# Kernel optimization log

Hardware: AMD Instinct MI355X
Metric: run time of the kernel (lower is better)

Reference implementation:

```python
import jax, jax.numpy as jnp
import numpy as np
from jax.scipy.stats import norm
from jax.scipy.special import ndtri

B, S, F = 512, 2048, 128

def setup_inputs() -> dict:
    key = jax.random.key(0)
    k1, k2, k3 = jax.random.split(key, 3)
    x = jax.random.normal(k1, (B, F), dtype=jnp.float32)
    cdf_data = jax.random.normal(k2, (S, F), dtype=jnp.float32)
    bw_param = jax.random.uniform(k3, (1, F), dtype=jnp.float32)
    return {"x": x, "cdf_data": cdf_data, "bw_param": bw_param}

def reference(x, cdf_data, bw_param):
    # trainable bandwidths: bw = sigmoid(raw param), shape [1, F]
    bw = jax.nn.sigmoid(bw_param)[0]  # [F]
    # Pairwise Gaussian-CDF KDE: for each (b, f), mean over stored samples s of
    # Phi((x[b,f] - cdf_data[s,f]) / bw[f]).  Intermediate z: [B, S, F].
    z = (x[:, None, :] - cdf_data[None, :, :]) / bw  # [B, S, F]
    u = jnp.mean(norm.cdf(z), axis=1)               # [B, F], uniform-ish in (0,1)
    # normal_backtransform=True: map uniform -> standard normal via inverse CDF
    return ndtri(u)
```

## Files before the change

kernel.cpp:

```cpp
#include <hip/hip_runtime.h>
#include <math.h>

#define FDIM  128
#define SDIM  2048
#define BDIM  512
#define GPTS  32
#define SP    32
#define PARTS 2
#define BLOCK1 (FDIM * PARTS)
#define XMIN  (-6.0)
#define XSPAN (12.0)
#define FG    2
#define BG    128
#define BLOCK2 256
#define PERF  (SP * GPTS)

__device__ __forceinline__ double ndtri_pair(double u, double cu) {
    double q = u - 0.5;
    if (fabs(q) <= 0.425) {
        double r = 0.180625 - q * q;
        double num = (((((((2.5090809287301226727e3  * r + 3.3430575583588128105e4) * r +
                            6.7265770927008700853e4) * r + 4.5921953931549871457e4) * r +
                            1.3731693765509461125e4) * r + 1.9715909503065514427e3) * r +
                            1.3314166789178437745e2) * r + 3.3871328727963666080e0);
        double den = (((((((5.2264952788528545610e3  * r + 2.8729085735721942674e4) * r +
                            3.9307895800092710610e4) * r + 2.1213794301586595867e4) * r +
                            5.3941960214247511077e3) * r + 6.8718700749205790830e2) * r +
                            4.2313330701600911252e1) * r + 1.0);
        return q * num / den;
    }
    double r = (q < 0.0) ? u : cu;
    r = fmax(r, 1e-300);
    r = sqrt(-log(r));
    double val;
    if (r <= 5.0) {
        r -= 1.6;
        double num = (((((((7.74545014278341407640e-4 * r + 2.27238449892691845833e-2) * r +
                            2.41780725177450611770e-1) * r + 1.27045825245236838258e0) * r +
                            3.64784832476320460504e0)  * r + 5.76949722146069140550e0) * r +
                            4.63033784615654529590e0)  * r + 1.42343711074968357734e0);
        double den = (((((((1.05075007164441684324e-9 * r + 5.47593808499534494600e-4) * r +
                            1.51986665636164571966e-2) * r + 1.48103976427480074590e-1) * r +
                            6.89767334985100004550e-1) * r + 1.67638483018380384940e0) * r +
                            2.05319162663775882187e0)  * r + 1.0);
        val = num / den;
    } else {
        r -= 5.0;
        double num = (((((((2.01033439929228813265e-7 * r + 2.71155556874348757815e-5) * r +
                            1.24266094738807843860e-3) * r + 2.65321895265761230930e-2) * r +
                            2.96560571828504891230e-1) * r + 1.78482653991729133580e0) * r +
                            5.46378491116411436990e0)  * r + 6.65790464350110377720e0);
        double den = (((((((2.04426310338993978564e-15 * r + 1.42151175831644588870e-7) * r +
                            1.84631831751005468180e-5)  * r + 7.86869131145613259100e-4) * r +
                            1.48753612908506148525e-2)  * r + 1.36929880922735805310e-1) * r +
                            5.99832206555887937690e-1)  * r + 1.0);
        val = num / den;
    }
    return (q < 0.0) ? -val : val;
}

__global__ __launch_bounds__(BLOCK1) void build_kernel(
    const float* __restrict__ cdf, const float* __restrict__ bwp,
    float2* __restrict__ part2)
{
    const int g    = blockIdx.x >> 5;
    const int sp   = blockIdx.x & (SP - 1);
    const int f    = threadIdx.x & (FDIM - 1);
    const int part = threadIdx.x >> 7;

    const float p = bwp[f];
    const float s = (1.0f + __expf(-p)) * 0.70710678118654752f;
    const float c1s    = 0.3275911f * s;
    const float negs2l = -(s * s) * 1.4426950408889634f;
    const float xg = (float)(XMIN + (double)g * (XSPAN / (GPTS - 1)));

    const int chunk = SDIM / SP / PARTS;
    const int base  = sp * (SDIM / SP) + part * chunk;
    const float* cp = cdf + base * FDIM + f;

    float acc0 = 0.f, acc1 = 0.f, acc2 = 0.f, acc3 = 0.f;
    float dac = 0.f;

    #pragma unroll 2
    for (int i = 0; i < chunk; i += 4) {
        float c0 = cp[0 * FDIM];
        float c1 = cp[1 * FDIM];
        float c2 = cp[2 * FDIM];
        float c3 = cp[3 * FDIM];
        cp += 4 * FDIM;

        float d0 = xg - c0, d1 = xg - c1, d2 = xg - c2, d3 = xg - c3;

        float t0 = __builtin_amdgcn_rcpf(fmaf(c1s, fabsf(d0), 1.0f));
        float t1 = __builtin_amdgcn_rcpf(fmaf(c1s, fabsf(d1), 1.0f));
        float t2 = __builtin_amdgcn_rcpf(fmaf(c1s, fabsf(d2), 1.0f));
        float t3 = __builtin_amdgcn_rcpf(fmaf(c1s, fabsf(d3), 1.0f));

        float x0 = exp2f(d0 * d0 * negs2l);
        float x1 = exp2f(d1 * d1 * negs2l);
        float x2 = exp2f(d2 * d2 * negs2l);
        float x3 = exp2f(d3 * d3 * negs2l);

        float q0 = fmaf(0.53070271450f, t0, -0.72657601350f);
        float q1 = fmaf(0.53070271450f, t1, -0.72657601350f);
        float q2 = fmaf(0.53070271450f, t2, -0.72657601350f);
        float q3 = fmaf(0.53070271450f, t3, -0.72657601350f);
        q0 = fmaf(q0, t0, 0.71070687050f);  q1 = fmaf(q1, t1, 0.71070687050f);
        q2 = fmaf(q2, t2, 0.71070687050f);  q3 = fmaf(q3, t3, 0.71070687050f);
        q0 = fmaf(q0, t0, -0.14224836800f); q1 = fmaf(q1, t1, -0.14224836800f);
        q2 = fmaf(q2, t2, -0.14224836800f); q3 = fmaf(q3, t3, -0.14224836800f);
        q0 = fmaf(q0, t0, 0.12741479600f);  q1 = fmaf(q1, t1, 0.12741479600f);
        q2 = fmaf(q2, t2, 0.12741479600f);  q3 = fmaf(q3, t3, 0.12741479600f);

        float e0 = q0 * t0 * x0;
        float e1 = q1 * t1 * x1;
        float e2 = q2 * t2 * x2;
        float e3 = q3 * t3 * x3;

        acc0 += (d0 >= 0.f) ? (1.0f - e0) : e0;
        acc1 += (d1 >= 0.f) ? (1.0f - e1) : e1;
        acc2 += (d2 >= 0.f) ? (1.0f - e2) : e2;
        acc3 += (d3 >= 0.f) ? (1.0f - e3) : e3;
        dac  += (x0 + x1) + (x2 + x3);
    }

    __shared__ float sacc[PARTS][FDIM];
    __shared__ float sdac[PARTS][FDIM];
    sacc[part][f] = (acc0 + acc1) + (acc2 + acc3);
    sdac[part][f] = dac;
    __syncthreads();

    if (part == 0) {
        float a  = sacc[0][f] + sacc[1][f];
        float da = sdac[0][f] + sdac[1][f];
        part2[f * PERF + sp * GPTS + g] = make_float2(a, da);
    }
}

__global__ __launch_bounds__(BLOCK2) void interp_kernel(
    const float* __restrict__ x, const float* __restrict__ bwp,
    const float2* __restrict__ part2, float* __restrict__ out)
{
    const int fg = blockIdx.x & 63;
    const int bg = blockIdx.x >> 6;
    const int F0 = fg * FG;
    const int B0 = bg * BG;
    const int tid = threadIdx.x;

    __shared__ float2 sp2[FG * PERF];
    __shared__ double tab[FG * GPTS][3];

    const float2* src = part2 + (size_t)F0 * PERF;
    #pragma unroll
    for (int k = tid; k < FG * PERF; k += BLOCK2) sp2[k] = src[k];
    __syncthreads();

    if (tid < FG * GPTS) {
        const int fi = tid >> 5;
        const int g  = tid & (GPTS - 1);
        double a = 0.0, da = 0.0;
        const int base = fi * PERF + g;
        #pragma unroll
        for (int sp = 0; sp < SP; ++sp) {
            float2 v = sp2[base + sp * GPTS];
            a  += (double)v.x;
            da += (double)v.y;
        }
        const double invS = 1.0 / (double)SDIM;
        const double invbw = 1.0 + exp(-(double)bwp[F0 + fi]);
        tab[tid][0] = a * invS;
        tab[tid][1] = ((double)SDIM - a) * invS;
        tab[tid][2] = da * invbw * (invS / 2.5066282746310002);
    }
    __syncthreads();

    const int bl = tid >> 1;
    const int fi = tid & 1;
    const int idx = (B0 + bl) * FDIM + F0 + fi;

    const double H = XSPAN / (GPTS - 1);
    double t = ((double)x[idx] - XMIN) * ((GPTS - 1) / XSPAN);
    t = fmin(fmax(t, 0.0), (double)(GPTS - 1));
    int i = (int)t;
    if (i > GPTS - 2) i = GPTS - 2;
    double w = t - (double)i;

    const int r0 = fi * GPTS + i;
    double u0 = tab[r0][0], u1 = tab[r0 + 1][0];
    double c0 = tab[r0][1], c1 = tab[r0 + 1][1];
    double m0 = tab[r0][2], m1 = tab[r0 + 1][2];

    double w2 = w * w, w3 = w2 * w;
    double h00 = 2.0 * w3 - 3.0 * w2 + 1.0;
    double h10 = w3 - 2.0 * w2 + w;
    double h01 = 3.0 * w2 - 2.0 * w3;
    double h11 = w3 - w2;
    double dterm = H * (h10 * m0 + h11 * m1);
    double u  = h00 * u0 + h01 * u1 + dterm;
    double cu = h00 * c0 + h01 * c1 - dterm;

    out[idx] = (float)ndtri_pair(u, cu);
}

extern "C" void kernel_launch(void* const* d_in, const int* in_sizes, int n_in,
                              void* d_out, int out_size, void* d_ws, size_t ws_size,
                              hipStream_t stream) {
    const float* x   = (const float*)d_in[0];
    const float* cdf = (const float*)d_in[1];
    const float* bwp = (const float*)d_in[2];
    float* out = (float*)d_out;

    float2* part2 = (float2*)d_ws;

    build_kernel<<<dim3(GPTS * SP), dim3(BLOCK1), 0, stream>>>(cdf, bwp, part2);
    interp_kernel<<<dim3((FDIM / FG) * (BDIM / BG)), dim3(BLOCK2), 0, stream>>>(
        x, bwp, part2, out);
}
```

Baseline: 67.11 us.

## Fuse build and interp kernels into one cooperative kernel with grid sync

```diff
diff --git a/kernel.cpp b/kernel.cpp
--- a/kernel.cpp
+++ b/kernel.cpp
@@ -1,19 +1,23 @@
 #include <hip/hip_runtime.h>
+#include <hip/hip_cooperative_groups.h>
 #include <math.h>
+
+namespace cg = cooperative_groups;
 
 #define FDIM  128
 #define SDIM  2048
 #define BDIM  512
 #define GPTS  32
-#define SP    32
+#define SPC   8
 #define PARTS 2
-#define BLOCK1 (FDIM * PARTS)
+#define CHUNK (SDIM / SPC / PARTS)
+#define NBLK  256
+#define NT    256
 #define XMIN  (-6.0)
 #define XSPAN (12.0)
 #define FG    2
 #define BG    128
-#define BLOCK2 256
-#define PERF  (SP * GPTS)
+#define PERF2 (SPC * GPTS)
 
 __device__ __forceinline__ double ndtri_pair(double u, double cu) {
     double q = u - 0.5;
@@ -59,110 +63,114 @@
     return (q < 0.0) ? -val : val;
 }
 
-__global__ __launch_bounds__(BLOCK1) void build_kernel(
-    const float* __restrict__ cdf, const float* __restrict__ bwp,
-    float2* __restrict__ part2)
+__global__ __launch_bounds__(NT) void fused_kernel(
+    const float* __restrict__ x, const float* __restrict__ cdf,
+    const float* __restrict__ bwp, float* out)
 {
-    const int g    = blockIdx.x >> 5;
-    const int sp   = blockIdx.x & (SP - 1);
-    const int f    = threadIdx.x & (FDIM - 1);
-    const int part = threadIdx.x >> 7;
-
-    const float p = bwp[f];
-    const float s = (1.0f + __expf(-p)) * 0.70710678118654752f;
-    const float c1s    = 0.3275911f * s;
-    const float negs2l = -(s * s) * 1.4426950408889634f;
-    const float xg = (float)(XMIN + (double)g * (XSPAN / (GPTS - 1)));
-
-    const int chunk = SDIM / SP / PARTS;
-    const int base  = sp * (SDIM / SP) + part * chunk;
-    const float* cp = cdf + base * FDIM + f;
-
-    float acc0 = 0.f, acc1 = 0.f, acc2 = 0.f, acc3 = 0.f;
-    float dac = 0.f;
-
-    #pragma unroll 2
-    for (int i = 0; i < chunk; i += 4) {
-        float c0 = cp[0 * FDIM];
-        float c1 = cp[1 * FDIM];
-        float c2 = cp[2 * FDIM];
-        float c3 = cp[3 * FDIM];
-        cp += 4 * FDIM;
-
-        float d0 = xg - c0, d1 = xg - c1, d2 = xg - c2, d3 = xg - c3;
-
-        float t0 = __builtin_amdgcn_rcpf(fmaf(c1s, fabsf(d0), 1.0f));
-        float t1 = __builtin_amdgcn_rcpf(fmaf(c1s, fabsf(d1), 1.0f));
-        float t2 = __builtin_amdgcn_rcpf(fmaf(c1s, fabsf(d2), 1.0f));
-        float t3 = __builtin_amdgcn_rcpf(fmaf(c1s, fabsf(d3), 1.0f));
-
-        float x0 = exp2f(d0 * d0 * negs2l);
-        float x1 = exp2f(d1 * d1 * negs2l);
-        float x2 = exp2f(d2 * d2 * negs2l);
-        float x3 = exp2f(d3 * d3 * negs2l);
-
-        float q0 = fmaf(0.53070271450f, t0, -0.72657601350f);
-        float q1 = fmaf(0.53070271450f, t1, -0.72657601350f);
-        float q2 = fmaf(0.53070271450f, t2, -0.72657601350f);
-        float q3 = fmaf(0.53070271450f, t3, -0.72657601350f);
-        q0 = fmaf(q0, t0, 0.71070687050f);  q1 = fmaf(q1, t1, 0.71070687050f);
-        q2 = fmaf(q2, t2, 0.71070687050f);  q3 = fmaf(q3, t3, 0.71070687050f);
-        q0 = fmaf(q0, t0, -0.14224836800f); q1 = fmaf(q1, t1, -0.14224836800f);
-        q2 = fmaf(q2, t2, -0.14224836800f); q3 = fmaf(q3, t3, -0.14224836800f);
-        q0 = fmaf(q0, t0, 0.12741479600f);  q1 = fmaf(q1, t1, 0.12741479600f);
-        q2 = fmaf(q2, t2, 0.12741479600f);  q3 = fmaf(q3, t3, 0.12741479600f);
-
-        float e0 = q0 * t0 * x0;
-        float e1 = q1 * t1 * x1;
-        float e2 = q2 * t2 * x2;
-        float e3 = q3 * t3 * x3;
-
-        acc0 += (d0 >= 0.f) ? (1.0f - e0) : e0;
-        acc1 += (d1 >= 0.f) ? (1.0f - e1) : e1;
-        acc2 += (d2 >= 0.f) ? (1.0f - e2) : e2;
-        acc3 += (d3 >= 0.f) ? (1.0f - e3) : e3;
-        dac  += (x0 + x1) + (x2 + x3);
-    }
-
-    __shared__ float sacc[PARTS][FDIM];
-    __shared__ float sdac[PARTS][FDIM];
-    sacc[part][f] = (acc0 + acc1) + (acc2 + acc3);
-    sdac[part][f] = dac;
-    __syncthreads();
-
-    if (part == 0) {
-        float a  = sacc[0][f] + sacc[1][f];
-        float da = sdac[0][f] + sdac[1][f];
-        part2[f * PERF + sp * GPTS + g] = make_float2(a, da);
-    }
-}
-
-__global__ __launch_bounds__(BLOCK2) void interp_kernel(
-    const float* __restrict__ x, const float* __restrict__ bwp,
-    const float2* __restrict__ part2, float* __restrict__ out)
-{
-    const int fg = blockIdx.x & 63;
-    const int bg = blockIdx.x >> 6;
+    float2* scratch = reinterpret_cast<float2*>(out);
+    const int tid = threadIdx.x;
+    const int blk = blockIdx.x;
+
+    __shared__ float  sacc[PARTS][FDIM];
+    __shared__ float  sdac[PARTS][FDIM];
+    __shared__ float2 sp2[FG * PERF2];
+    __shared__ double tab[FG * GPTS][3];
+
+    {
+        const int g    = blk & (GPTS - 1);
+        const int sp   = blk >> 5;
+        const int f    = tid & (FDIM - 1);
+        const int part = tid >> 7;
+
+        const float p = bwp[f];
+        const float s = (1.0f + __expf(-p)) * 0.70710678118654752f;
+        const float c1s    = 0.3275911f * s;
+        const float negs2l = -(s * s) * 1.4426950408889634f;
+        const float xg = (float)(XMIN + (double)g * (XSPAN / (GPTS - 1)));
+
+        const int base = sp * (SDIM / SPC) + part * CHUNK;
+        const float* cp = cdf + (size_t)base * FDIM + f;
+
+        float acc0 = 0.f, acc1 = 0.f, acc2 = 0.f, acc3 = 0.f;
+        float dac = 0.f;
+
+        #pragma unroll 2
+        for (int i = 0; i < CHUNK; i += 4) {
+            float c0 = cp[0 * FDIM];
+            float c1 = cp[1 * FDIM];
+            float c2 = cp[2 * FDIM];
+            float c3 = cp[3 * FDIM];
+            cp += 4 * FDIM;
+
+            float d0 = xg - c0, d1 = xg - c1, d2 = xg - c2, d3 = xg - c3;
+
+            float t0 = __builtin_amdgcn_rcpf(fmaf(c1s, fabsf(d0), 1.0f));
+            float t1 = __builtin_amdgcn_rcpf(fmaf(c1s, fabsf(d1), 1.0f));
+            float t2 = __builtin_amdgcn_rcpf(fmaf(c1s, fabsf(d2), 1.0f));
+            float t3 = __builtin_amdgcn_rcpf(fmaf(c1s, fabsf(d3), 1.0f));
+
+            float x0 = exp2f(d0 * d0 * negs2l);
+            float x1 = exp2f(d1 * d1 * negs2l);
+            float x2 = exp2f(d2 * d2 * negs2l);
+            float x3 = exp2f(d3 * d3 * negs2l);
+
+            float q0 = fmaf(0.53070271450f, t0, -0.72657601350f);
+            float q1 = fmaf(0.53070271450f, t1, -0.72657601350f);
+            float q2 = fmaf(0.53070271450f, t2, -0.72657601350f);
+            float q3 = fmaf(0.53070271450f, t3, -0.72657601350f);
+            q0 = fmaf(q0, t0, 0.71070687050f);  q1 = fmaf(q1, t1, 0.71070687050f);
+            q2 = fmaf(q2, t2, 0.71070687050f);  q3 = fmaf(q3, t3, 0.71070687050f);
+            q0 = fmaf(q0, t0, -0.14224836800f); q1 = fmaf(q1, t1, -0.14224836800f);
+            q2 = fmaf(q2, t2, -0.14224836800f); q3 = fmaf(q3, t3, -0.14224836800f);
+            q0 = fmaf(q0, t0, 0.12741479600f);  q1 = fmaf(q1, t1, 0.12741479600f);
+            q2 = fmaf(q2, t2, 0.12741479600f);  q3 = fmaf(q3, t3, 0.12741479600f);
+
+            float e0 = q0 * t0 * x0;
+            float e1 = q1 * t1 * x1;
+            float e2 = q2 * t2 * x2;
+            float e3 = q3 * t3 * x3;
+
+            acc0 += (d0 >= 0.f) ? (1.0f - e0) : e0;
+            acc1 += (d1 >= 0.f) ? (1.0f - e1) : e1;
+            acc2 += (d2 >= 0.f) ? (1.0f - e2) : e2;
+            acc3 += (d3 >= 0.f) ? (1.0f - e3) : e3;
+            dac  += (x0 + x1) + (x2 + x3);
+        }
+
+        sacc[part][f] = (acc0 + acc1) + (acc2 + acc3);
+        sdac[part][f] = dac;
+        __syncthreads();
+
+        if (part == 0) {
+            float a  = sacc[0][f] + sacc[1][f];
+            float da = sdac[0][f] + sdac[1][f];
+            scratch[(size_t)f * PERF2 + sp * GPTS + g] = make_float2(a, da);
+        }
+    }
+
+    cg::this_grid().sync();
+
+    const int fg = blk & 63;
+    const int bg = blk >> 6;
     const int F0 = fg * FG;
     const int B0 = bg * BG;
-    const int tid = threadIdx.x;
-
-    __shared__ float2 sp2[FG * PERF];
-    __shared__ double tab[FG * GPTS][3];
-
-    const float2* src = part2 + (size_t)F0 * PERF;
-    #pragma unroll
-    for (int k = tid; k < FG * PERF; k += BLOCK2) sp2[k] = src[k];
-    __syncthreads();
+
+    {
+        const float2* src = scratch + (size_t)F0 * PERF2;
+        #pragma unroll
+        for (int k = tid; k < FG * PERF2; k += NT) sp2[k] = src[k];
+    }
+
+    cg::this_grid().sync();
 
     if (tid < FG * GPTS) {
         const int fi = tid >> 5;
         const int g  = tid & (GPTS - 1);
         double a = 0.0, da = 0.0;
-        const int base = fi * PERF + g;
+        const int baseq = fi * PERF2 + g;
         #pragma unroll
-        for (int sp = 0; sp < SP; ++sp) {
-            float2 v = sp2[base + sp * GPTS];
+        for (int sp = 0; sp < SPC; ++sp) {
+            float2 v = sp2[baseq + sp * GPTS];
             a  += (double)v.x;
             da += (double)v.y;
         }
@@ -210,9 +218,7 @@
     const float* bwp = (const float*)d_in[2];
     float* out = (float*)d_out;
 
-    float2* part2 = (float2*)d_ws;
-
-    build_kernel<<<dim3(GPTS * SP), dim3(BLOCK1), 0, stream>>>(cdf, bwp, part2);
-    interp_kernel<<<dim3((FDIM / FG) * (BDIM / BG)), dim3(BLOCK2), 0, stream>>>(
-        x, bwp, part2, out);
+    void* args[] = { (void*)&x, (void*)&cdf, (void*)&bwp, (void*)&out };
+    hipLaunchCooperativeKernel(fused_kernel, dim3(NBLK), dim3(NT),
+                               args, 0, stream);
 }
```

Measured after the change: 139.7 us. 108% more time.
